# Optimization experiments

Measured on AMD Instinct MI355X. Metric: run time of the kernel, lower is better.

The kernel has to match this reference:

```python
import jax, jax.numpy as jnp
import numpy as np

N = 50000      # nodes
E = 1600000    # edges (avg degree 32)
IN = 64        # in_dim
EIN = 32       # edge_in_dim
H = 4          # num_heads
D = 16         # out_dim per head
ALPHA = 0.2    # leaky relu slope


def setup_inputs() -> dict:
    key = jax.random.key(0)
    ks = jax.random.split(key, 12)
    s = 0.05  # small init scale, mimics xavier gain=0.1
    return {
        "x": jax.random.normal(ks[0], (N, IN), dtype=jnp.float32),
        "e": jax.random.normal(ks[1], (E, EIN), dtype=jnp.float32),
        "src": jax.random.randint(ks[2], (E,), 0, N, dtype=jnp.int32),
        "dst": jax.random.randint(ks[3], (E,), 0, N, dtype=jnp.int32),
        "W": jax.random.normal(ks[4], (IN, H * D), dtype=jnp.float32) * s,
        "b": jax.random.normal(ks[5], (H * D,), dtype=jnp.float32) * s,
        "We": jax.random.normal(ks[6], (EIN, H * D), dtype=jnp.float32) * s,
        "be": jax.random.normal(ks[7], (H * D,), dtype=jnp.float32) * s,
        "attn_l": jax.random.normal(ks[8], (H, D), dtype=jnp.float32) * s,
        "attn_r": jax.random.normal(ks[9], (H, D), dtype=jnp.float32) * s,
        "attn_e": jax.random.normal(ks[10], (EIN, H), dtype=jnp.float32) * s,
    }


def reference(x, e, src, dst, W, b, We, be, attn_l, attn_r, attn_e):
    # node transform: [N, H, D]
    ft = (x @ W + b).reshape(N, H, D)
    # per-node attention halves: [N, H]
    a1 = jnp.einsum("nhd,hd->nh", ft, attn_l)
    a2 = jnp.einsum("nhd,hd->nh", ft, attn_r)
    # per-edge attention term: [E, H]
    a3 = e @ attn_e
    # edge attention logits (leaky relu): [E, H]
    a = a1[src] + a2[dst] + a3
    a = jnp.where(a > 0, a, ALPHA * a)
    # edge softmax over incoming edges of each dst node (max-stabilized)
    m = jax.ops.segment_max(a, dst, num_segments=N)          # [N, H]
    scores = jnp.exp(a - m[dst])                              # [E, H]
    z = jax.ops.segment_sum(scores, dst, num_segments=N)     # [N, H]
    # weighted feature aggregation: sum_e scores * ft[src] -> [N, H, D]
    ft_agg = jax.ops.segment_sum(scores[:, :, None] * ft[src], dst, num_segments=N)
    # transformed edge features aggregated per dst: [N, H*D] -> [N, H, D]
    eft = e @ We + be
    sum_eft = jax.ops.segment_sum(eft, dst, num_segments=N).reshape(N, H, D)
    ret = ft_agg / z[:, :, None] + sum_eft
    return ret.reshape(N, H * D)
```

## Files before the change

kernel.cpp:

```cpp
#include <hip/hip_runtime.h>

#define ALPHA 0.2f

constexpr int IN  = 64;
constexpr int EIN = 32;
constexpr int H   = 4;
constexpr int D   = 16;
constexpr int HD  = 64;
constexpr int MAXDEG = 96;

struct alignas(32) Rec { int eid; int srcn; float sc[4]; int pad[2]; };

__global__ __launch_bounds__(256) void node_v2_kernel(
    const float* __restrict__ x, const float* __restrict__ W,
    const float* __restrict__ b, const float* __restrict__ attn_l,
    const float* __restrict__ attn_r,
    float* __restrict__ ft, float* __restrict__ a1, float* __restrict__ a2,
    int N) {
  __shared__ float xs[64][68];
  __shared__ float Ws[64][64];
  int tid = threadIdx.x;
  int nbase = blockIdx.x * 64;
  for (int i = tid; i < 1024; i += 256)
    ((float4*)Ws)[i] = ((const float4*)W)[i];
  for (int i = tid; i < 1024; i += 256) {
    int node = i >> 4;
    int k4 = (i & 15) * 4;
    int gn = nbase + node;
    float4 v = make_float4(0.f, 0.f, 0.f, 0.f);
    if (gn < N) v = ((const float4*)(x + (size_t)gn * IN))[i & 15];
    xs[k4 + 0][node] = v.x; xs[k4 + 1][node] = v.y;
    xs[k4 + 2][node] = v.z; xs[k4 + 3][node] = v.w;
  }
  __syncthreads();
  int cg = tid & 15, ng = tid >> 4;
  float4 bv = ((const float4*)b)[cg];
  float acc[4][4];
  #pragma unroll
  for (int ni = 0; ni < 4; ++ni) {
    acc[ni][0] = bv.x; acc[ni][1] = bv.y; acc[ni][2] = bv.z; acc[ni][3] = bv.w;
  }
  #pragma unroll 8
  for (int k = 0; k < 64; ++k) {
    float4 wv = *(const float4*)&Ws[k][cg * 4];
    float4 xv = *(const float4*)&xs[k][ng * 4];
    const float* wp = &wv.x;
    const float* xp = &xv.x;
    #pragma unroll
    for (int ni = 0; ni < 4; ++ni)
      #pragma unroll
      for (int c = 0; c < 4; ++c)
        acc[ni][c] += xp[ni] * wp[c];
  }
  __syncthreads();
  #pragma unroll
  for (int ni = 0; ni < 4; ++ni) {
    int node = ng * 4 + ni;
    float4 o = make_float4(acc[ni][0], acc[ni][1], acc[ni][2], acc[ni][3]);
    *(float4*)&xs[node][cg * 4] = o;
    int gn = nbase + node;
    if (gn < N) ((float4*)(ft + (size_t)gn * HD))[cg] = o;
  }
  __syncthreads();
  int node = tid >> 2, h = tid & 3;
  int gn = nbase + node;
  if (gn < N) {
    float p1 = 0.f, p2 = 0.f;
    #pragma unroll
    for (int d4 = 0; d4 < 4; ++d4) {
      float4 fv = *(const float4*)&xs[node][h * 16 + d4 * 4];
      float4 lv = ((const float4*)attn_l)[h * 4 + d4];
      float4 rv = ((const float4*)attn_r)[h * 4 + d4];
      p1 += fv.x * lv.x + fv.y * lv.y + fv.z * lv.z + fv.w * lv.w;
      p2 += fv.x * rv.x + fv.y * rv.y + fv.z * rv.z + fv.w * rv.w;
    }
    a1[(size_t)gn * H + h] = p1;
    a2[(size_t)gn * H + h] = p2;
  }
}

__global__ __launch_bounds__(256) void edge_ell_kernel(
    const float* __restrict__ e, const int* __restrict__ src,
    const int* __restrict__ dst, const float* __restrict__ attn_e,
    const float* __restrict__ a1, const float* __restrict__ a2,
    int* __restrict__ cnt, Rec* __restrict__ ell, int E) {
  __shared__ float Ael[EIN * H];
  int tid = threadIdx.x;
  if (tid < EIN * H) Ael[tid] = attn_e[tid];
  __syncthreads();
  int i = blockIdx.x * 256 + tid;
  if (i >= E) return;
  int d = dst[i], s = src[i];
  const float4* e4 = (const float4*)(e + (size_t)i * EIN);
  float a3h[H] = {0.f, 0.f, 0.f, 0.f};
  #pragma unroll
  for (int j = 0; j < 8; ++j) {
    float4 v = e4[j];
    const float* vp = &v.x;
    #pragma unroll
    for (int t = 0; t < 4; ++t) {
      float ek = vp[t];
      int k = j * 4 + t;
      #pragma unroll
      for (int h = 0; h < H; ++h) a3h[h] += ek * Ael[k * H + h];
    }
  }
  float4 av1 = ((const float4*)a1)[s];
  float4 av2 = ((const float4*)a2)[d];
  const float* p1 = &av1.x;
  const float* p2 = &av2.x;
  float o[H];
  #pragma unroll
  for (int h = 0; h < H; ++h) {
    float a = p1[h] + p2[h] + a3h[h];
    a = a > 0.f ? a : ALPHA * a;
    o[h] = __expf(a);
  }
  int slot = atomicAdd(&cnt[d], 1);
  if (slot < MAXDEG) {
    float4* rp = (float4*)(ell + (size_t)d * MAXDEG + slot);
    rp[0] = make_float4(__int_as_float(i), __int_as_float(s), o[0], o[1]);
    rp[1] = make_float4(o[2], o[3], 0.f, 0.f);
  }
}

__global__ __launch_bounds__(256) void agg_ell_kernel(
    const float* __restrict__ e, const float* __restrict__ ft,
    const int* __restrict__ cnt, const Rec* __restrict__ ell,
    const float* __restrict__ We, const float* __restrict__ be,
    float* __restrict__ out, int N) {
  __shared__ float Wel[EIN * HD];
  __shared__ float bel[HD];
  int tid = threadIdx.x;
  for (int i = tid; i < EIN * HD; i += 256) Wel[i] = We[i];
  if (tid < HD) bel[tid] = be[tid];
  __syncthreads();
  int lane = tid & 63, wid = tid >> 6;
  int n = blockIdx.x * 4 + wid;
  if (n >= N) return;
  int deg = cnt[n];
  deg = deg < MAXDEG ? deg : MAXDEG;
  const Rec* row = ell + (size_t)n * MAXDEG;
  int h  = lane >> 4;
  int ke = lane & 31;
  float acc = 0.f, z = 0.f, esum = 0.f;
  int i = 0;
  for (; i + 8 <= deg; i += 8) {
    int eidv[8], srcv[8];
    float scv[8], ev[8], fv[8];
    #pragma unroll
    for (int u = 0; u < 8; ++u) {
      const Rec* r = row + i + u;
      eidv[u] = r->eid;
      srcv[u] = r->srcn;
      scv[u]  = r->sc[h];
    }
    #pragma unroll
    for (int u = 0; u < 8; ++u) ev[u] = e[(size_t)eidv[u] * EIN + ke];
    #pragma unroll
    for (int u = 0; u < 8; ++u) fv[u] = ft[(size_t)srcv[u] * HD + lane];
    #pragma unroll
    for (int u = 0; u < 8; ++u) {
      acc += scv[u] * fv[u];
      z += scv[u];
      esum += ev[u];
    }
  }
  for (; i < deg; ++i) {
    const Rec* r = row + i;
    float sc = r->sc[h];
    float ev = e[(size_t)r->eid * EIN + ke];
    float fv = ft[(size_t)r->srcn * HD + lane];
    acc += sc * fv;
    z += sc;
    esum += ev;
  }
  float sacc = 0.f;
  #pragma unroll
  for (int k = 0; k < EIN; ++k) {
    float ekk = __shfl(esum, k);
    sacc += ekk * Wel[k * HD + lane];
  }
  float agg = (z > 0.f) ? acc / z : 0.f;
  out[(size_t)n * HD + lane] = agg + sacc + (float)deg * bel[lane];
}

extern "C" void kernel_launch(void* const* d_in, const int* in_sizes, int n_in,
                              void* d_out, int out_size, void* d_ws, size_t ws_size,
                              hipStream_t stream) {
  const float* x      = (const float*)d_in[0];
  const float* e      = (const float*)d_in[1];
  const int*   src    = (const int*)d_in[2];
  const int*   dst    = (const int*)d_in[3];
  const float* W      = (const float*)d_in[4];
  const float* b      = (const float*)d_in[5];
  const float* We     = (const float*)d_in[6];
  const float* be     = (const float*)d_in[7];
  const float* attn_l = (const float*)d_in[8];
  const float* attn_r = (const float*)d_in[9];
  const float* attn_e = (const float*)d_in[10];
  float* out = (float*)d_out;
  int N = in_sizes[0] / IN;
  int E = in_sizes[1] / EIN;

  char* w = (char*)d_ws;
  float* ft  = (float*)w; w += (size_t)N * HD * 4;
  float* a1  = (float*)w; w += (size_t)N * H * 4;
  float* a2  = (float*)w; w += (size_t)N * H * 4;
  int*   cnt = (int*)w;   w += (size_t)N * 4;
  Rec*   ell = (Rec*)w;   w += (size_t)N * MAXDEG * sizeof(Rec);

  hipMemsetAsync(cnt, 0, (size_t)N * sizeof(int), stream);

  node_v2_kernel<<<(N + 63) / 64, 256, 0, stream>>>(
      x, W, b, attn_l, attn_r, ft, a1, a2, N);
  edge_ell_kernel<<<(E + 255) / 256, 256, 0, stream>>>(
      e, src, dst, attn_e, a1, a2, cnt, ell, E);
  agg_ell_kernel<<<(N + 3) / 4, 256, 0, stream>>>(
      e, ft, cnt, ell, We, be, out, N);
}
```

Before: 547.9 us.

## Pack edge scores as bf16 into 16-byte ELL records and add nontemporal loads

Shrinks each ELL record from 32 to 16 bytes by storing the four per-head exp scores as bf16 pairs. This halves the scattered write traffic in the edge kernel and the record reads in the aggregation kernel. It also marks streaming loads of e, src, dst and x as nontemporal and has each edge block process two edges per thread. The cost is lower score precision, which affects both the softmax numerator and its normaliser.

```diff
diff --git a/kernel.cpp b/kernel.cpp
--- a/kernel.cpp
+++ b/kernel.cpp
@@ -9,7 +9,22 @@
 constexpr int HD  = 64;
 constexpr int MAXDEG = 96;
 
-struct alignas(32) Rec { int eid; int srcn; float sc[4]; int pad[2]; };
+typedef float f32x4 __attribute__((ext_vector_type(4)));
+
+struct alignas(16) Rec { int eid; int srcn; unsigned s01; unsigned s23; };
+
+__device__ inline unsigned pack_bf16x2(float lo, float hi) {
+  unsigned a = __float_as_uint(lo), b = __float_as_uint(hi);
+  a = (a + 0x7FFFu + ((a >> 16) & 1u)) >> 16;
+  b = (b + 0x7FFFu + ((b >> 16) & 1u)) >> 16;
+  return a | (b << 16);
+}
+
+__device__ inline float unpack_sc(unsigned s01, unsigned s23, int h) {
+  unsigned w = (h & 2) ? s23 : s01;
+  unsigned half = (h & 1) ? (w >> 16) : (w & 0xFFFFu);
+  return __uint_as_float(half << 16);
+}
 
 __global__ __launch_bounds__(256) void node_v2_kernel(
     const float* __restrict__ x, const float* __restrict__ W,
@@ -27,8 +42,8 @@
     int node = i >> 4;
     int k4 = (i & 15) * 4;
     int gn = nbase + node;
-    float4 v = make_float4(0.f, 0.f, 0.f, 0.f);
-    if (gn < N) v = ((const float4*)(x + (size_t)gn * IN))[i & 15];
+    f32x4 v = {0.f, 0.f, 0.f, 0.f};
+    if (gn < N) v = __builtin_nontemporal_load(((const f32x4*)(x + (size_t)gn * IN)) + (i & 15));
     xs[k4 + 0][node] = v.x; xs[k4 + 1][node] = v.y;
     xs[k4 + 2][node] = v.z; xs[k4 + 3][node] = v.w;
   }
@@ -88,39 +103,45 @@
   int tid = threadIdx.x;
   if (tid < EIN * H) Ael[tid] = attn_e[tid];
   __syncthreads();
-  int i = blockIdx.x * 256 + tid;
-  if (i >= E) return;
-  int d = dst[i], s = src[i];
-  const float4* e4 = (const float4*)(e + (size_t)i * EIN);
-  float a3h[H] = {0.f, 0.f, 0.f, 0.f};
-  #pragma unroll
-  for (int j = 0; j < 8; ++j) {
-    float4 v = e4[j];
-    const float* vp = &v.x;
-    #pragma unroll
-    for (int t = 0; t < 4; ++t) {
-      float ek = vp[t];
-      int k = j * 4 + t;
+  int base = blockIdx.x * 512;
+  #pragma unroll
+  for (int half = 0; half < 2; ++half) {
+    int i = base + half * 256 + tid;
+    if (i >= E) continue;
+    int d = __builtin_nontemporal_load(dst + i);
+    int s = __builtin_nontemporal_load(src + i);
+    const f32x4* e4 = (const f32x4*)(e + (size_t)i * EIN);
+    float a3h[H] = {0.f, 0.f, 0.f, 0.f};
+    #pragma unroll
+    for (int j = 0; j < 8; ++j) {
+      f32x4 v = __builtin_nontemporal_load(e4 + j);
       #pragma unroll
-      for (int h = 0; h < H; ++h) a3h[h] += ek * Ael[k * H + h];
-    }
-  }
-  float4 av1 = ((const float4*)a1)[s];
-  float4 av2 = ((const float4*)a2)[d];
-  const float* p1 = &av1.x;
-  const float* p2 = &av2.x;
-  float o[H];
-  #pragma unroll
-  for (int h = 0; h < H; ++h) {
-    float a = p1[h] + p2[h] + a3h[h];
-    a = a > 0.f ? a : ALPHA * a;
-    o[h] = __expf(a);
-  }
-  int slot = atomicAdd(&cnt[d], 1);
-  if (slot < MAXDEG) {
-    float4* rp = (float4*)(ell + (size_t)d * MAXDEG + slot);
-    rp[0] = make_float4(__int_as_float(i), __int_as_float(s), o[0], o[1]);
-    rp[1] = make_float4(o[2], o[3], 0.f, 0.f);
+      for (int t = 0; t < 4; ++t) {
+        float ek = v[t];
+        int k = j * 4 + t;
+        #pragma unroll
+        for (int h = 0; h < H; ++h) a3h[h] += ek * Ael[k * H + h];
+      }
+    }
+    float4 av1 = ((const float4*)a1)[s];
+    float4 av2 = ((const float4*)a2)[d];
+    const float* p1 = &av1.x;
+    const float* p2 = &av2.x;
+    float o[H];
+    #pragma unroll
+    for (int h = 0; h < H; ++h) {
+      float a = p1[h] + p2[h] + a3h[h];
+      a = a > 0.f ? a : ALPHA * a;
+      o[h] = __expf(a);
+    }
+    int slot = atomicAdd(&cnt[d], 1);
+    if (slot < MAXDEG) {
+      Rec r;
+      r.eid = i; r.srcn = s;
+      r.s01 = pack_bf16x2(o[0], o[1]);
+      r.s23 = pack_bf16x2(o[2], o[3]);
+      *(Rec*)(ell + (size_t)d * MAXDEG + slot) = r;
+    }
   }
 }
 
@@ -140,25 +161,24 @@
   if (n >= N) return;
   int deg = cnt[n];
   deg = deg < MAXDEG ? deg : MAXDEG;
-  const Rec* row = ell + (size_t)n * MAXDEG;
+  const int4* row = (const int4*)(ell + (size_t)n * MAXDEG);
   int h  = lane >> 4;
   int ke = lane & 31;
   float acc = 0.f, z = 0.f, esum = 0.f;
   int i = 0;
   for (; i + 8 <= deg; i += 8) {
-    int eidv[8], srcv[8];
+    int4 rec[8];
     float scv[8], ev[8], fv[8];
     #pragma unroll
-    for (int u = 0; u < 8; ++u) {
-      const Rec* r = row + i + u;
-      eidv[u] = r->eid;
-      srcv[u] = r->srcn;
-      scv[u]  = r->sc[h];
-    }
-    #pragma unroll
-    for (int u = 0; u < 8; ++u) ev[u] = e[(size_t)eidv[u] * EIN + ke];
-    #pragma unroll
-    for (int u = 0; u < 8; ++u) fv[u] = ft[(size_t)srcv[u] * HD + lane];
+    for (int u = 0; u < 8; ++u) rec[u] = row[i + u];
+    #pragma unroll
+    for (int u = 0; u < 8; ++u)
+      ev[u] = __builtin_nontemporal_load(e + (size_t)rec[u].x * EIN + ke);
+    #pragma unroll
+    for (int u = 0; u < 8; ++u) fv[u] = ft[(size_t)rec[u].y * HD + lane];
+    #pragma unroll
+    for (int u = 0; u < 8; ++u)
+      scv[u] = unpack_sc((unsigned)rec[u].z, (unsigned)rec[u].w, h);
     #pragma unroll
     for (int u = 0; u < 8; ++u) {
       acc += scv[u] * fv[u];
@@ -167,10 +187,10 @@
     }
   }
   for (; i < deg; ++i) {
-    const Rec* r = row + i;
-    float sc = r->sc[h];
-    float ev = e[(size_t)r->eid * EIN + ke];
-    float fv = ft[(size_t)r->srcn * HD + lane];
+    int4 r = row[i];
+    float sc = unpack_sc((unsigned)r.z, (unsigned)r.w, h);
+    float ev = __builtin_nontemporal_load(e + (size_t)r.x * EIN + ke);
+    float fv = ft[(size_t)r.y * HD + lane];
     acc += sc * fv;
     z += sc;
     esum += ev;
@@ -210,11 +230,11 @@
   int*   cnt = (int*)w;   w += (size_t)N * 4;
   Rec*   ell = (Rec*)w;   w += (size_t)N * MAXDEG * sizeof(Rec);
 
-  hipMemsetAsync(cnt, 0, (size_t)N * sizeof(int), stream);
+  (void)hipMemsetAsync(cnt, 0, (size_t)N * sizeof(int), stream);
 
   node_v2_kernel<<<(N + 63) / 64, 256, 0, stream>>>(
       x, W, b, attn_l, attn_r, ft, a1, a2, N);
-  edge_ell_kernel<<<(E + 255) / 256, 256, 0, stream>>>(
+  edge_ell_kernel<<<(E + 511) / 512, 256, 0, stream>>>(
       e, src, dst, attn_e, a1, a2, cnt, ell, E);
   agg_ell_kernel<<<(N + 3) / 4, 256, 0, stream>>>(
       e, ft, cnt, ell, We, be, out, N);
```

Result: slower. 610.9 us (+11.5%).

## Fuse edge attention scoring into aggregation kernel, shrink ELL records to int2

Applied to the files above, without the earlier changes.

The per-edge attention logit computation (e·attn_e, leaky relu, exp) moves out of the edge scatter kernel and into the per-node aggregation kernel. There it uses DPP reductions and bpermute to share scores across lanes, processing 4 edges per iteration. The scatter kernel now writes only (edge id, src) pairs instead of 32-byte records. This removes one full read of the edge features and the larger ELL write and read traffic, at the cost of more cross-lane shuffle work inside the aggregation loop.

```diff
diff --git a/kernel.cpp b/kernel.cpp
--- a/kernel.cpp
+++ b/kernel.cpp
@@ -9,7 +9,23 @@
 constexpr int HD  = 64;
 constexpr int MAXDEG = 96;
 
-struct alignas(32) Rec { int eid; int srcn; float sc[4]; int pad[2]; };
+typedef float f32x4 __attribute__((ext_vector_type(4)));
+
+template <int CTRL>
+__device__ inline float dpp_add(float v) {
+  int r = __builtin_amdgcn_update_dpp(0, __float_as_int(v), CTRL, 0xF, 0xF, false);
+  return v + __int_as_float(r);
+}
+__device__ inline float red16(float v) {
+  v = dpp_add<0x121>(v);
+  v = dpp_add<0x122>(v);
+  v = dpp_add<0x124>(v);
+  v = dpp_add<0x128>(v);
+  return v;
+}
+__device__ inline float bpermf(int byte_addr, float v) {
+  return __int_as_float(__builtin_amdgcn_ds_bpermute(byte_addr, __float_as_int(v)));
+}
 
 __global__ __launch_bounds__(256) void node_v2_kernel(
     const float* __restrict__ x, const float* __restrict__ W,
@@ -27,8 +43,8 @@
     int node = i >> 4;
     int k4 = (i & 15) * 4;
     int gn = nbase + node;
-    float4 v = make_float4(0.f, 0.f, 0.f, 0.f);
-    if (gn < N) v = ((const float4*)(x + (size_t)gn * IN))[i & 15];
+    f32x4 v = {0.f, 0.f, 0.f, 0.f};
+    if (gn < N) v = *(((const f32x4*)(x + (size_t)gn * IN)) + (i & 15));
     xs[k4 + 0][node] = v.x; xs[k4 + 1][node] = v.y;
     xs[k4 + 2][node] = v.z; xs[k4 + 3][node] = v.w;
   }
@@ -79,54 +95,26 @@
   }
 }
 
-__global__ __launch_bounds__(256) void edge_ell_kernel(
-    const float* __restrict__ e, const int* __restrict__ src,
-    const int* __restrict__ dst, const float* __restrict__ attn_e,
+__global__ __launch_bounds__(256) void fill_kernel(
+    const int* __restrict__ src, const int* __restrict__ dst,
+    int* __restrict__ cnt, int2* __restrict__ ell, int E) {
+  int base = blockIdx.x * 1024 + threadIdx.x;
+  #pragma unroll
+  for (int u = 0; u < 4; ++u) {
+    int i = base + u * 256;
+    if (i < E) {
+      int d = dst[i], s = src[i];
+      int slot = atomicAdd(&cnt[d], 1);
+      if (slot < MAXDEG) ell[(size_t)d * MAXDEG + slot] = make_int2(i, s);
+    }
+  }
+}
+
+__global__ __launch_bounds__(256) void agg_fused_kernel(
+    const float* __restrict__ e, const float* __restrict__ ft,
     const float* __restrict__ a1, const float* __restrict__ a2,
-    int* __restrict__ cnt, Rec* __restrict__ ell, int E) {
-  __shared__ float Ael[EIN * H];
-  int tid = threadIdx.x;
-  if (tid < EIN * H) Ael[tid] = attn_e[tid];
-  __syncthreads();
-  int i = blockIdx.x * 256 + tid;
-  if (i >= E) return;
-  int d = dst[i], s = src[i];
-  const float4* e4 = (const float4*)(e + (size_t)i * EIN);
-  float a3h[H] = {0.f, 0.f, 0.f, 0.f};
-  #pragma unroll
-  for (int j = 0; j < 8; ++j) {
-    float4 v = e4[j];
-    const float* vp = &v.x;
-    #pragma unroll
-    for (int t = 0; t < 4; ++t) {
-      float ek = vp[t];
-      int k = j * 4 + t;
-      #pragma unroll
-      for (int h = 0; h < H; ++h) a3h[h] += ek * Ael[k * H + h];
-    }
-  }
-  float4 av1 = ((const float4*)a1)[s];
-  float4 av2 = ((const float4*)a2)[d];
-  const float* p1 = &av1.x;
-  const float* p2 = &av2.x;
-  float o[H];
-  #pragma unroll
-  for (int h = 0; h < H; ++h) {
-    float a = p1[h] + p2[h] + a3h[h];
-    a = a > 0.f ? a : ALPHA * a;
-    o[h] = __expf(a);
-  }
-  int slot = atomicAdd(&cnt[d], 1);
-  if (slot < MAXDEG) {
-    float4* rp = (float4*)(ell + (size_t)d * MAXDEG + slot);
-    rp[0] = make_float4(__int_as_float(i), __int_as_float(s), o[0], o[1]);
-    rp[1] = make_float4(o[2], o[3], 0.f, 0.f);
-  }
-}
-
-__global__ __launch_bounds__(256) void agg_ell_kernel(
-    const float* __restrict__ e, const float* __restrict__ ft,
-    const int* __restrict__ cnt, const Rec* __restrict__ ell,
+    const float* __restrict__ attn_e,
+    const int* __restrict__ cnt, const int2* __restrict__ ell,
     const float* __restrict__ We, const float* __restrict__ be,
     float* __restrict__ out, int N) {
   __shared__ float Wel[EIN * HD];
@@ -138,43 +126,63 @@
   int lane = tid & 63, wid = tid >> 6;
   int n = blockIdx.x * 4 + wid;
   if (n >= N) return;
+  int grp = lane >> 4;
+  int kk  = lane & 15;
+  int hsel = kk & 3;
   int deg = cnt[n];
   deg = deg < MAXDEG ? deg : MAXDEG;
-  const Rec* row = ell + (size_t)n * MAXDEG;
-  int h  = lane >> 4;
-  int ke = lane & 31;
-  float acc = 0.f, z = 0.f, esum = 0.f;
-  int i = 0;
-  for (; i + 8 <= deg; i += 8) {
-    int eidv[8], srcv[8];
-    float scv[8], ev[8], fv[8];
-    #pragma unroll
-    for (int u = 0; u < 8; ++u) {
-      const Rec* r = row + i + u;
-      eidv[u] = r->eid;
-      srcv[u] = r->srcn;
-      scv[u]  = r->sc[h];
+  const int2* row = ell + (size_t)n * MAXDEG;
+  float4 aeA = ((const float4*)attn_e)[kk];
+  float4 aeB = ((const float4*)attn_e)[kk + 16];
+  float a2sel = a2[(size_t)n * H + hsel];
+  int bp0 = (0 * 16 + grp) * 4, bp1 = (1 * 16 + grp) * 4;
+  int bp2 = (2 * 16 + grp) * 4, bp3 = (3 * 16 + grp) * 4;
+  float acc = 0.f, z = 0.f, es0 = 0.f, es1 = 0.f;
+  for (int i = 0; i < deg; i += 4) {
+    int rem = deg - i;
+    int i1 = rem > 1 ? i + 1 : i;
+    int i2 = rem > 2 ? i + 2 : i;
+    int i3 = rem > 3 ? i + 3 : i;
+    int2 r0 = row[i], r1 = row[i1], r2 = row[i2], r3 = row[i3];
+    int eidu = (grp & 2) ? ((grp & 1) ? r3.x : r2.x) : ((grp & 1) ? r1.x : r0.x);
+    int srcu = (grp & 2) ? ((grp & 1) ? r3.y : r2.y) : ((grp & 1) ? r1.y : r0.y);
+    const float* erow = e + (size_t)eidu * EIN;
+    float ev0 = erow[kk];
+    float ev1 = erow[kk + 16];
+    float p0 = ev0 * aeA.x + ev1 * aeB.x;
+    float p1 = ev0 * aeA.y + ev1 * aeB.y;
+    float p2 = ev0 * aeA.z + ev1 * aeB.z;
+    float p3 = ev0 * aeA.w + ev1 * aeB.w;
+    p0 = red16(p0); p1 = red16(p1); p2 = red16(p2); p3 = red16(p3);
+    float psel = (hsel & 2) ? ((hsel & 1) ? p3 : p2) : ((hsel & 1) ? p1 : p0);
+    float a1v = a1[(size_t)srcu * H + hsel];
+    float lg = a1v + a2sel + psel;
+    lg = lg > 0.f ? lg : ALPHA * lg;
+    float sc = __expf(lg);
+    float vs0 = bpermf(bp0, sc);
+    float vs1 = bpermf(bp1, sc);
+    float vs2 = bpermf(bp2, sc);
+    float vs3 = bpermf(bp3, sc);
+    if (rem < 4) {
+      vs1 = rem > 1 ? vs1 : 0.f;
+      vs2 = rem > 2 ? vs2 : 0.f;
+      vs3 = rem > 3 ? vs3 : 0.f;
     }
-    #pragma unroll
-    for (int u = 0; u < 8; ++u) ev[u] = e[(size_t)eidv[u] * EIN + ke];
-    #pragma unroll
-    for (int u = 0; u < 8; ++u) fv[u] = ft[(size_t)srcv[u] * HD + lane];
-    #pragma unroll
-    for (int u = 0; u < 8; ++u) {
-      acc += scv[u] * fv[u];
-      z += scv[u];
-      esum += ev[u];
-    }
-  }
-  for (; i < deg; ++i) {
-    const Rec* r = row + i;
-    float sc = r->sc[h];
-    float ev = e[(size_t)r->eid * EIN + ke];
-    float fv = ft[(size_t)r->srcn * HD + lane];
-    acc += sc * fv;
-    z += sc;
-    esum += ev;
-  }
+    float ft0 = ft[(size_t)r0.y * HD + lane];
+    float ft1 = ft[(size_t)r1.y * HD + lane];
+    float ft2 = ft[(size_t)r2.y * HD + lane];
+    float ft3 = ft[(size_t)r3.y * HD + lane];
+    acc += vs0 * ft0; acc += vs1 * ft1; acc += vs2 * ft2; acc += vs3 * ft3;
+    z += vs0 + vs1 + vs2 + vs3;
+    bool gvalid = grp < rem;
+    es0 += gvalid ? ev0 : 0.f;
+    es1 += gvalid ? ev1 : 0.f;
+  }
+  float t0 = es0 + bpermf((lane ^ 16) << 2, es0);
+  t0 = t0 + bpermf((lane ^ 32) << 2, t0);
+  float t1 = es1 + bpermf((lane ^ 16) << 2, es1);
+  t1 = t1 + bpermf((lane ^ 32) << 2, t1);
+  float esum = (lane & 16) ? t1 : t0;
   float sacc = 0.f;
   #pragma unroll
   for (int k = 0; k < EIN; ++k) {
@@ -208,14 +216,13 @@
   float* a1  = (float*)w; w += (size_t)N * H * 4;
   float* a2  = (float*)w; w += (size_t)N * H * 4;
   int*   cnt = (int*)w;   w += (size_t)N * 4;
-  Rec*   ell = (Rec*)w;   w += (size_t)N * MAXDEG * sizeof(Rec);
-
-  hipMemsetAsync(cnt, 0, (size_t)N * sizeof(int), stream);
+  int2*  ell = (int2*)w;  w += (size_t)N * MAXDEG * 8;
+
+  (void)hipMemsetAsync(cnt, 0, (size_t)N * sizeof(int), stream);
 
   node_v2_kernel<<<(N + 63) / 64, 256, 0, stream>>>(
       x, W, b, attn_l, attn_r, ft, a1, a2, N);
-  edge_ell_kernel<<<(E + 255) / 256, 256, 0, stream>>>(
-      e, src, dst, attn_e, a1, a2, cnt, ell, E);
-  agg_ell_kernel<<<(N + 3) / 4, 256, 0, stream>>>(
-      e, ft, cnt, ell, We, be, out, N);
-}
+  fill_kernel<<<(E + 1023) / 1024, 256, 0, stream>>>(src, dst, cnt, ell, E);
+  agg_fused_kernel<<<(N + 3) / 4, 256, 0, stream>>>(
+      e, ft, a1, a2, attn_e, cnt, ell, We, be, out, N);
+}
```

Result: no change. 543.2 us (-0.9%).
